# Performance work log

Hardware: AMD Instinct MI355X
Metric: run time of the kernel (lower is better)

Reference implementation:

```python
import jax, jax.numpy as jnp
import numpy as np

B, S, D, H = 4, 1024, 1024, 16
HD = D // H  # head_dim = 64


def setup_inputs() -> dict:
    key = jax.random.key(0)
    ks = jax.random.split(key, 16)
    w = lambda k: jax.random.normal(k, (D, D), dtype=jnp.float32) * 0.02
    b = lambda k: jax.random.normal(k, (D,), dtype=jnp.float32) * 0.02
    x = jax.random.normal(ks[0], (B, S, D), dtype=jnp.float32)
    mask = jnp.tril(jnp.ones((S, S), dtype=jnp.int32))[None, None]  # causal [1,1,S,S]
    bar_indices = jax.random.randint(ks[1], (S,), 0, S, dtype=jnp.int64)
    beat_indices = jax.random.randint(ks[2], (S,), 0, S, dtype=jnp.int64)
    return {
        "x": x, "mask": mask, "bar_indices": bar_indices, "beat_indices": beat_indices,
        "Wq": w(ks[3]), "bq": b(ks[4]), "Wk": w(ks[5]), "bk": b(ks[6]),
        "Wv": w(ks[7]), "bv": b(ks[8]),
        "W_bark": w(ks[9]), "b_bark": b(ks[10]),
        "W_beatk": w(ks[11]), "b_beatk": b(ks[12]),
        "Wo": w(ks[13]), "bo": b(ks[14]),
    }


def reference(x, mask, bar_indices, beat_indices, Wq, bq, Wk, bk, Wv, bv,
              W_bark, b_bark, W_beatk, b_beatk, Wo, bo):
    Bs, Sl, Dm = x.shape
    heads, hd = H, Dm // H

    def proj(t, W, b):  # torch Linear: t @ W.T + b, then split heads -> [B,H,S,hd]
        y = t @ W.T + b
        return y.reshape(Bs, -1, heads, hd).transpose(0, 2, 1, 3)

    q = proj(x, Wq, bq)
    k = proj(x, Wk, bk)
    v = proj(x, Wv, bv)
    scale = 1.0 / jnp.sqrt(jnp.asarray(hd, x.dtype))

    scores = jnp.einsum('bhqd,bhkd->bhqk', q, k) * scale

    # hierarchical bar bias (bar_query is computed but unused in the original)
    bar_k = proj(x[:, bar_indices], W_bark, b_bark)
    scores = scores + 0.2 * (jnp.einsum('bhqd,bhkd->bhqk', q, bar_k) * scale)

    # hierarchical beat bias
    beat_k = proj(x[:, beat_indices], W_beatk, b_beatk)
    scores = scores + 0.1 * (jnp.einsum('bhqd,bhkd->bhqk', q, beat_k) * scale)

    scores = jnp.where(mask == 0, jnp.asarray(-1e9, scores.dtype), scores)
    attn = jax.nn.softmax(scores, axis=-1)  # dropout is identity in eval

    out = jnp.einsum('bhqk,bhkd->bhqd', attn, v)
    out = out.transpose(0, 2, 1, 3).reshape(Bs, Sl, Dm)
    return out @ Wo.T + bo
```

## Files before the change

### kernel.cpp

```cpp
#include <hip/hip_runtime.h>
#include <hip/hip_bf16.h>


typedef __bf16 bf16x8 __attribute__((ext_vector_type(8)));
typedef __bf16 bf16x4 __attribute__((ext_vector_type(4)));
typedef float  f32x4  __attribute__((ext_vector_type(4)));

#define DMODEL 1024

#define ASYNC_LOAD16(gp, lp)                                                  \
    __builtin_amdgcn_global_load_lds(                                         \
        (const __attribute__((address_space(1))) unsigned int*)(gp),          \
        (__attribute__((address_space(3))) unsigned int*)(lp), 16, 0, 0)

__global__ __launch_bounds__(256) void cvt_kernel(
    const float* __restrict__ x,
    const float* __restrict__ Wq, const float* __restrict__ Wk,
    const float* __restrict__ Wv, const float* __restrict__ Wbar,
    const float* __restrict__ Wbeat, const float* __restrict__ Wo,
    __bf16* __restrict__ dst)
{
    const int g = blockIdx.x * 256 + threadIdx.x;
    const size_t e = (size_t)g * 8;
    const int seg = (int)(e >> 20);
    const float* src; size_t off; float s = 1.0f;
    if (seg < 4)       { src = x;     off = e; }
    else if (seg == 4) { src = Wq;    off = e - ((size_t)4 << 20); }
    else if (seg == 5) { src = Wk;    off = e - ((size_t)5 << 20); }
    else if (seg == 6) { src = Wv;    off = e - ((size_t)6 << 20); }
    else if (seg == 7) { src = Wbar;  off = e - ((size_t)7 << 20); s = 0.2f; }
    else if (seg == 8) { src = Wbeat; off = e - ((size_t)8 << 20); s = 0.1f; }
    else               { src = Wo;    off = e - ((size_t)9 << 20); }
    const float4 a = *(const float4*)&src[off];
    const float4 b = *(const float4*)&src[off + 4];
    bf16x8 v;
    v[0] = (__bf16)(a.x * s); v[1] = (__bf16)(a.y * s);
    v[2] = (__bf16)(a.z * s); v[3] = (__bf16)(a.w * s);
    v[4] = (__bf16)(b.x * s); v[5] = (__bf16)(b.y * s);
    v[6] = (__bf16)(b.z * s); v[7] = (__bf16)(b.w * s);
    *(bf16x8*)&dst[e] = v;
}

__global__ __launch_bounds__(256) void proj_kernel(
    const __bf16* __restrict__ xb, const __bf16* __restrict__ attnbuf,
    const __bf16* __restrict__ Wqb, const __bf16* __restrict__ Wkb,
    const __bf16* __restrict__ Wvb, const __bf16* __restrict__ Wbarb,
    const __bf16* __restrict__ Wbeatb, const __bf16* __restrict__ Wob,
    const float* __restrict__ bq, const float* __restrict__ bk,
    const float* __restrict__ bv, const float* __restrict__ bbar,
    const float* __restrict__ bbeat, const float* __restrict__ bo,
    const int* __restrict__ bar_idx, const int* __restrict__ beat_idx,
    __bf16* __restrict__ qbuf, __bf16* __restrict__ keffbuf,
    __bf16* __restrict__ vtbuf, float* __restrict__ outbuf,
    int mode_base)
{
    const int mode = mode_base + blockIdx.y;
    const int tile = blockIdx.x;
    const int m0 = (tile >> 3) << 7;
    const int n0 = (tile & 7) << 7;

    __shared__ __align__(16) __bf16 Alds[128 * 32];
    __shared__ __align__(16) __bf16 Blds[128 * 32];

    const int t    = threadIdx.x;
    const int w    = t >> 6;
    const int lane = t & 63;
    const int l15  = lane & 15;
    const int quad = lane >> 4;
    const int wm   = (w >> 1) << 6;
    const int wn   = (w & 1) << 6;
    const int srow = t >> 2;
    const int scol = (t & 3) * 8;

    const __bf16* Aptr = (mode == 3) ? attnbuf : xb;
    const int nterms = (mode == 1) ? 3 : 1;

    f32x4 acc[4][4];
    for (int i = 0; i < 4; ++i)
        for (int j = 0; j < 4; ++j)
            acc[i][j] = {0.f, 0.f, 0.f, 0.f};

    for (int term = 0; term < nterms; ++term) {
        const __bf16* Wterm =
            (mode == 0) ? Wqb :
            (mode == 2) ? Wvb :
            (mode == 3) ? Wob :
            (term == 0) ? Wkb : (term == 1) ? Wbarb : Wbeatb;

        int arow0, arow1;
        if (mode != 1 || term == 0) {
            arow0 = m0 + srow;
            arow1 = m0 + 64 + srow;
        } else {
            const int* gi = (term == 1) ? bar_idx : beat_idx;
            const int bbase = m0 & ~1023;
            arow0 = bbase + gi[(m0 & 1023) + srow];
            arow1 = bbase + gi[(m0 & 1023) + 64 + srow];
        }
        const __bf16* gA0 = Aptr + (size_t)arow0 * DMODEL + scol;
        const __bf16* gA1 = Aptr + (size_t)arow1 * DMODEL + scol;
        const __bf16* gB0 = Wterm + (size_t)(n0 + srow) * DMODEL + scol;
        const __bf16* gB1 = Wterm + (size_t)(n0 + 64 + srow) * DMODEL + scol;
        __bf16* lA0 = &Alds[w * 512];
        __bf16* lA1 = &Alds[2048 + w * 512];
        __bf16* lB0 = &Blds[w * 512];
        __bf16* lB1 = &Blds[2048 + w * 512];

        for (int kk = 0; kk < 32; ++kk) {
            const int k0 = kk * 32;
            ASYNC_LOAD16(gA0 + k0, lA0);
            ASYNC_LOAD16(gA1 + k0, lA1);
            ASYNC_LOAD16(gB0 + k0, lB0);
            ASYNC_LOAD16(gB1 + k0, lB1);
            __syncthreads();

            bf16x8 af[4], bfr[4];
            for (int i = 0; i < 4; ++i)
                af[i] = *(const bf16x8*)&Alds[(wm + i * 16 + l15) * 32 + quad * 8];
            for (int j = 0; j < 4; ++j)
                bfr[j] = *(const bf16x8*)&Blds[(wn + j * 16 + l15) * 32 + quad * 8];

            for (int i = 0; i < 4; ++i)
                for (int j = 0; j < 4; ++j)
                    acc[i][j] = __builtin_amdgcn_mfma_f32_16x16x32_bf16(
                        af[i], bfr[j], acc[i][j], 0, 0, 0);
            __syncthreads();
        }
    }

    for (int j = 0; j < 4; ++j) {
        const int col = n0 + wn + j * 16 + l15;
        float bias;
        if (mode == 0)      bias = bq[col];
        else if (mode == 1) bias = bk[col] + 0.2f * bbar[col] + 0.1f * bbeat[col];
        else if (mode == 2) bias = bv[col];
        else                bias = bo[col];

        for (int i = 0; i < 4; ++i) {
            const int rowbase = m0 + wm + i * 16 + quad * 4;
            if (mode == 2) {
                const int bb = rowbase >> 10;
                const int sb = rowbase & 1023;
                bf16x4 vv;
                for (int r = 0; r < 4; ++r) vv[r] = (__bf16)(acc[i][j][r] + bias);
                *(bf16x4*)&vtbuf[((size_t)(bb * 1024 + col)) * 1024 + sb] = vv;
            } else if (mode == 3) {
                for (int r = 0; r < 4; ++r)
                    outbuf[(size_t)(rowbase + r) * DMODEL + col] =
                        acc[i][j][r] + bias;
            } else if (mode == 0) {
                for (int r = 0; r < 4; ++r)
                    qbuf[(size_t)(rowbase + r) * DMODEL + col] =
                        (__bf16)((acc[i][j][r] + bias) * 0.125f);
            } else {
                for (int r = 0; r < 4; ++r)
                    keffbuf[(size_t)(rowbase + r) * DMODEL + col] =
                        (__bf16)(acc[i][j][r] + bias);
            }
        }
    }
}

__global__ __launch_bounds__(256) void oproj_kernel(
    const __bf16* __restrict__ attnb, const __bf16* __restrict__ Wob,
    const float* __restrict__ bo, float* __restrict__ outb)
{
    const int tile = blockIdx.x;
    const int m0 = (tile >> 3) << 6;
    const int n0 = (tile & 7) << 7;

    __shared__ __align__(16) __bf16 Alds[64 * 32];
    __shared__ __align__(16) __bf16 Blds[128 * 32];

    const int t    = threadIdx.x;
    const int w    = t >> 6;
    const int lane = t & 63;
    const int l15  = lane & 15;
    const int quad = lane >> 4;
    const int wm   = (w >> 1) << 5;
    const int wn   = (w & 1) << 6;
    const int srow = t >> 2;
    const int scol = (t & 3) * 8;

    const __bf16* gA  = attnb + (size_t)(m0 + srow) * DMODEL + scol;
    const __bf16* gB0 = Wob + (size_t)(n0 + srow) * DMODEL + scol;
    const __bf16* gB1 = Wob + (size_t)(n0 + 64 + srow) * DMODEL + scol;
    __bf16* lA  = &Alds[w * 512];
    __bf16* lB0 = &Blds[w * 512];
    __bf16* lB1 = &Blds[2048 + w * 512];

    f32x4 acc[2][4];
    for (int i = 0; i < 2; ++i)
        for (int j = 0; j < 4; ++j)
            acc[i][j] = {0.f, 0.f, 0.f, 0.f};

    for (int kk = 0; kk < 32; ++kk) {
        const int k0 = kk * 32;
        ASYNC_LOAD16(gA + k0, lA);
        ASYNC_LOAD16(gB0 + k0, lB0);
        ASYNC_LOAD16(gB1 + k0, lB1);
        __syncthreads();

        bf16x8 af[2], bfr[4];
        for (int i = 0; i < 2; ++i)
            af[i] = *(const bf16x8*)&Alds[(wm + i * 16 + l15) * 32 + quad * 8];
        for (int j = 0; j < 4; ++j)
            bfr[j] = *(const bf16x8*)&Blds[(wn + j * 16 + l15) * 32 + quad * 8];

        for (int i = 0; i < 2; ++i)
            for (int j = 0; j < 4; ++j)
                acc[i][j] = __builtin_amdgcn_mfma_f32_16x16x32_bf16(
                    af[i], bfr[j], acc[i][j], 0, 0, 0);
        __syncthreads();
    }

    for (int j = 0; j < 4; ++j) {
        const int col = n0 + wn + j * 16 + l15;
        const float bias = bo[col];
        for (int i = 0; i < 2; ++i) {
            const int rowbase = m0 + wm + i * 16 + quad * 4;
            for (int r = 0; r < 4; ++r)
                outb[(size_t)(rowbase + r) * DMODEL + col] = acc[i][j][r] + bias;
        }
    }
}

__global__ __launch_bounds__(256) void attn_kernel(
    const __bf16* __restrict__ qbuf, const __bf16* __restrict__ keffbuf,
    const __bf16* __restrict__ vtbuf, __bf16* __restrict__ attnbuf)
{
    const int bh = blockIdx.y;
    const int b  = bh >> 4;
    const int h  = bh & 15;
    const int qt = blockIdx.x;
    const int q0 = qt * 64;

    __shared__ __align__(16) __bf16 Klds[64][72];
    __shared__ __align__(16) __bf16 Vlds[64][72];
    __shared__ __align__(16) __bf16 Plds[4][16][72];

    const int t    = threadIdx.x;
    const int w    = t >> 6;
    const int lane = t & 63;
    const int l15  = lane & 15;
    const int quad = lane >> 4;

    const __bf16* qbase =
        qbuf + (size_t)(b * 1024 + q0 + w * 16 + l15) * DMODEL + h * 64;
    bf16x8 qf0 = *(const bf16x8*)&qbase[quad * 8];
    bf16x8 qf1 = *(const bf16x8*)&qbase[32 + quad * 8];

    bf16x8 ones;
    for (int i = 0; i < 8; ++i) ones[i] = (__bf16)1.0f;

    f32x4 o[4];
    for (int i = 0; i < 4; ++i) o[i] = {0.f, 0.f, 0.f, 0.f};
    f32x4 lacc = {0.f, 0.f, 0.f, 0.f};

    const int srow = t >> 2;
    const int scol = (t & 3) * 16;

    const __bf16* kbase = keffbuf + (size_t)(b * 1024) * DMODEL + h * 64;
    const __bf16* vtb   = vtbuf + (size_t)(b * 1024 + h * 64) * 1024;

    for (int j = 0; j <= qt; ++j) {
        const __bf16* kg = kbase + (size_t)(j * 64 + srow) * DMODEL + scol;
        *(bf16x8*)&Klds[srow][scol]     = *(const bf16x8*)kg;
        *(bf16x8*)&Klds[srow][scol + 8] = *(const bf16x8*)(kg + 8);
        const __bf16* vg = vtb + (size_t)srow * 1024 + j * 64 + scol;
        *(bf16x8*)&Vlds[srow][scol]     = *(const bf16x8*)vg;
        *(bf16x8*)&Vlds[srow][scol + 8] = *(const bf16x8*)(vg + 8);
        __syncthreads();

        f32x4 sc[4];
        for (int nt = 0; nt < 4; ++nt) {
            sc[nt] = {0.f, 0.f, 0.f, 0.f};
            bf16x8 kf0 = *(const bf16x8*)&Klds[nt * 16 + l15][quad * 8];
            bf16x8 kf1 = *(const bf16x8*)&Klds[nt * 16 + l15][32 + quad * 8];
            sc[nt] = __builtin_amdgcn_mfma_f32_16x16x32_bf16(qf0, kf0, sc[nt], 0, 0, 0);
            sc[nt] = __builtin_amdgcn_mfma_f32_16x16x32_bf16(qf1, kf1, sc[nt], 0, 0, 0);
        }

        if (j == qt) {
            const int qrow_base = q0 + w * 16 + quad * 4;
            for (int nt = 0; nt < 4; ++nt) {
                const int kcol = j * 64 + nt * 16 + l15;
                for (int r = 0; r < 4; ++r)
                    if (kcol > qrow_base + r) sc[nt][r] = -1e30f;
            }
        }

        for (int nt = 0; nt < 4; ++nt)
            for (int r = 0; r < 4; ++r)
                sc[nt][r] = __expf(sc[nt][r]);

        for (int nt = 0; nt < 4; ++nt)
            for (int r = 0; r < 4; ++r)
                Plds[w][quad * 4 + r][nt * 16 + l15] = (__bf16)sc[nt][r];
        asm volatile("s_waitcnt lgkmcnt(0)" ::: "memory");

        bf16x8 pf0 = *(const bf16x8*)&Plds[w][l15][quad * 8];
        bf16x8 pf1 = *(const bf16x8*)&Plds[w][l15][32 + quad * 8];

        lacc = __builtin_amdgcn_mfma_f32_16x16x32_bf16(pf0, ones, lacc, 0, 0, 0);
        lacc = __builtin_amdgcn_mfma_f32_16x16x32_bf16(pf1, ones, lacc, 0, 0, 0);

        for (int nd = 0; nd < 4; ++nd) {
            bf16x8 vf0 = *(const bf16x8*)&Vlds[nd * 16 + l15][quad * 8];
            bf16x8 vf1 = *(const bf16x8*)&Vlds[nd * 16 + l15][32 + quad * 8];
            o[nd] = __builtin_amdgcn_mfma_f32_16x16x32_bf16(pf0, vf0, o[nd], 0, 0, 0);
            o[nd] = __builtin_amdgcn_mfma_f32_16x16x32_bf16(pf1, vf1, o[nd], 0, 0, 0);
        }
        __syncthreads();
    }

    float rinv[4];
    for (int r = 0; r < 4; ++r) rinv[r] = 1.0f / lacc[r];
    for (int nd = 0; nd < 4; ++nd) {
        for (int r = 0; r < 4; ++r) {
            const int row = q0 + w * 16 + quad * 4 + r;
            attnbuf[(size_t)(b * 1024 + row) * DMODEL + h * 64 + nd * 16 + l15] =
                (__bf16)(o[nd][r] * rinv[r]);
        }
    }
}

extern "C" void kernel_launch(void* const* d_in, const int* in_sizes, int n_in,
                              void* d_out, int out_size, void* d_ws, size_t ws_size,
                              hipStream_t stream) {
    const float* x     = (const float*)d_in[0];
    const int* bar     = (const int*)d_in[2];
    const int* beat    = (const int*)d_in[3];
    const float* Wq    = (const float*)d_in[4];
    const float* bq    = (const float*)d_in[5];
    const float* Wk    = (const float*)d_in[6];
    const float* bk    = (const float*)d_in[7];
    const float* Wv    = (const float*)d_in[8];
    const float* bv    = (const float*)d_in[9];
    const float* Wbar  = (const float*)d_in[10];
    const float* bbar  = (const float*)d_in[11];
    const float* Wbeat = (const float*)d_in[12];
    const float* bbeat = (const float*)d_in[13];
    const float* Wo    = (const float*)d_in[14];
    const float* bo    = (const float*)d_in[15];

    const size_t M1 = (size_t)1 << 20;
    __bf16* xb     = (__bf16*)d_ws;
    __bf16* Wqb    = xb + 4 * M1;
    __bf16* Wkb    = Wqb + M1;
    __bf16* Wvb    = Wkb + M1;
    __bf16* Wbarb  = Wvb + M1;
    __bf16* Wbeatb = Wbarb + M1;
    __bf16* Wob    = Wbeatb + M1;
    __bf16* qbuf   = Wob + M1;
    __bf16* keff   = qbuf + 4 * M1;
    __bf16* vt     = keff + 4 * M1;
    __bf16* attn   = vt + 4 * M1;
    float*  outb   = (float*)d_out;

    cvt_kernel<<<5120, 256, 0, stream>>>(x, Wq, Wk, Wv, Wbar, Wbeat, Wo, xb);

    proj_kernel<<<dim3(256, 3), 256, 0, stream>>>(
        xb, attn, Wqb, Wkb, Wvb, Wbarb, Wbeatb, Wob,
        bq, bk, bv, bbar, bbeat, bo, bar, beat,
        qbuf, keff, vt, outb, 0);

    attn_kernel<<<dim3(16, 64), 256, 0, stream>>>(qbuf, keff, vt, attn);

    oproj_kernel<<<512, 256, 0, stream>>>(attn, Wob, bo, outb);
}
```

Measured before the change: 237.5 us.

## Replace projection GEMM with double-buffered 8-wave 128x256 tile kernel

Swaps the simple single-buffered 128x128 projection GEMM for a 512-thread kernel with 128x256 tiles, BK=64, double-buffered LDS, XOR-swizzled layout and a four-phase interleaving of async global-to-LDS loads with MFMA bursts. Longer-running K-effective blocks (48 k-steps) are scheduled first. The goal is to hide global memory latency, cut LDS bank conflicts and per-kstep barrier overhead in the Q/Keff/V projections. It relies on hand-placed vmcnt waits and barriers being correct, and uses much more LDS per block (96 KB), which may limit occupancy.

```diff
diff --git a/kernel.cpp b/kernel.cpp
--- a/kernel.cpp
+++ b/kernel.cpp
@@ -41,121 +41,235 @@
     *(bf16x8*)&dst[e] = v;
 }
 
-__global__ __launch_bounds__(256) void proj_kernel(
-    const __bf16* __restrict__ xb, const __bf16* __restrict__ attnbuf,
+
+#define SWZ_COL(r_, ks_) \
+    (((((ks_) * 64) + quad * 16) ^ ((((r_) >> 2) & 1) << 5)) >> 1)
+
+#define READ_A(c_, mh_)                                                       \
+    do {                                                                      \
+        _Pragma("unroll") for (int mi = 0; mi < 2; ++mi) {                    \
+            const int r_ = ((w >> 2) << 5) + (mh_) * 64 + mi * 16 + l15;      \
+            _Pragma("unroll") for (int ks = 0; ks < 2; ++ks)                  \
+                af[mi][ks] = *(const bf16x8*)&Alds[(c_) * 8192 + r_ * 64 +    \
+                                                   SWZ_COL(r_, ks)];          \
+        }                                                                     \
+    } while (0)
+
+#define READ_B(c_, nh_)                                                       \
+    do {                                                                      \
+        _Pragma("unroll") for (int nj = 0; nj < 2; ++nj) {                    \
+            const int r_ = ((w & 3) << 5) + (nh_) * 128 + nj * 16 + l15;      \
+            _Pragma("unroll") for (int ks = 0; ks < 2; ++ks)                  \
+                bf[nj][ks] = *(const bf16x8*)&Blds[(c_) * 16384 + r_ * 64 +   \
+                                                    SWZ_COL(r_, ks)];         \
+        }                                                                     \
+    } while (0)
+
+#define STAGE_A8(bufn_, h_, kt_)                                              \
+    do {                                                                      \
+        const int tm_ = (kt_) >> 4;                                           \
+        const int k0_ = ((kt_) & 15) << 6;                                    \
+        const __bf16* ap_ = (tm_ == 0) ? aA0##h_ : (tm_ == 1) ? aA1##h_       \
+                                                              : aA2##h_;      \
+        ASYNC_LOAD16(ap_ + k0_,                                               \
+                     &Alds[(bufn_) * 8192 + (h_) * 4096 + w * 512]);          \
+    } while (0)
+
+#define STAGE_B8(bufn_, h_, kt_)                                              \
+    do {                                                                      \
+        const int tm_ = (kt_) >> 4;                                           \
+        const int k0_ = ((kt_) & 15) << 6;                                    \
+        const __bf16* wp_ = (tm_ == 0) ? W0 : (tm_ == 1) ? W1 : W2;           \
+        ASYNC_LOAD16(wp_ + bro##h_##0 + k0_,                                  \
+                     &Blds[(bufn_) * 16384 + (h_) * 8192 + w * 512]);         \
+        ASYNC_LOAD16(wp_ + bro##h_##1 + k0_,                                  \
+                     &Blds[(bufn_) * 16384 + (h_) * 8192 + 4096 + w * 512]);  \
+    } while (0)
+
+#define PHASE_BAR1()                                                          \
+    do {                                                                      \
+        __builtin_amdgcn_s_barrier();                                         \
+        asm volatile("s_waitcnt lgkmcnt(0)" ::: "memory");                    \
+    } while (0)
+
+#define MFMA8(mh_, nh_)                                                       \
+    do {                                                                      \
+        __builtin_amdgcn_s_setprio(1);                                        \
+        _Pragma("unroll") for (int mi = 0; mi < 2; ++mi)                      \
+        _Pragma("unroll") for (int nj = 0; nj < 2; ++nj) {                    \
+            acc[(mh_)*2 + mi][(nh_)*2 + nj] =                                 \
+                __builtin_amdgcn_mfma_f32_16x16x32_bf16(                      \
+                    af[mi][0], bf[nj][0], acc[(mh_)*2 + mi][(nh_)*2 + nj],    \
+                    0, 0, 0);                                                 \
+            acc[(mh_)*2 + mi][(nh_)*2 + nj] =                                 \
+                __builtin_amdgcn_mfma_f32_16x16x32_bf16(                      \
+                    af[mi][1], bf[nj][1], acc[(mh_)*2 + mi][(nh_)*2 + nj],    \
+                    0, 0, 0);                                                 \
+        }                                                                     \
+        __builtin_amdgcn_s_setprio(0);                                        \
+    } while (0)
+
+__global__ __launch_bounds__(512, 2) void gemm8p_kernel(
+    const __bf16* __restrict__ xb,
     const __bf16* __restrict__ Wqb, const __bf16* __restrict__ Wkb,
     const __bf16* __restrict__ Wvb, const __bf16* __restrict__ Wbarb,
-    const __bf16* __restrict__ Wbeatb, const __bf16* __restrict__ Wob,
+    const __bf16* __restrict__ Wbeatb,
     const float* __restrict__ bq, const float* __restrict__ bk,
     const float* __restrict__ bv, const float* __restrict__ bbar,
-    const float* __restrict__ bbeat, const float* __restrict__ bo,
+    const float* __restrict__ bbeat,
     const int* __restrict__ bar_idx, const int* __restrict__ beat_idx,
     __bf16* __restrict__ qbuf, __bf16* __restrict__ keffbuf,
-    __bf16* __restrict__ vtbuf, float* __restrict__ outbuf,
-    int mode_base)
+    __bf16* __restrict__ vtbuf)
 {
-    const int mode = mode_base + blockIdx.y;
-    const int tile = blockIdx.x;
-    const int m0 = (tile >> 3) << 7;
-    const int n0 = (tile & 7) << 7;
-
-    __shared__ __align__(16) __bf16 Alds[128 * 32];
-    __shared__ __align__(16) __bf16 Blds[128 * 32];
-
-    const int t    = threadIdx.x;
+    __shared__ __align__(16) __bf16 Alds[2 * 8192];
+    __shared__ __align__(16) __bf16 Blds[2 * 16384];
+
+    const int bid = blockIdx.x;
+    int mode, tk;
+    if (bid < 128)      { mode = 1; tk = bid; }
+    else if (bid < 256) { mode = 0; tk = bid - 128; }
+    else                { mode = 2; tk = bid - 256; }
+    const int m0 = (tk >> 2) << 7;
+    const int n0 = (tk & 3) << 8;
+    const int nkt = (mode == 1) ? 48 : 16;
+
+    const int t    = (int)threadIdx.x;
     const int w    = t >> 6;
     const int lane = t & 63;
     const int l15  = lane & 15;
     const int quad = lane >> 4;
-    const int wm   = (w >> 1) << 6;
-    const int wn   = (w & 1) << 6;
-    const int srow = t >> 2;
-    const int scol = (t & 3) * 8;
-
-    const __bf16* Aptr = (mode == 3) ? attnbuf : xb;
-    const int nterms = (mode == 1) ? 3 : 1;
+
+    const int srow = t >> 3;
+    const int scol = ((((t & 7) * 16) ^ (((t >> 5) & 1) << 5)) >> 1);
+
+    const __bf16* aA00 = xb + (size_t)(m0 + srow) * DMODEL + scol;
+    const __bf16* aA01 = xb + (size_t)(m0 + 64 + srow) * DMODEL + scol;
+    const __bf16* aA10 = aA00; const __bf16* aA11 = aA01;
+    const __bf16* aA20 = aA00; const __bf16* aA21 = aA01;
+    const __bf16 *W0, *W1, *W2;
+    if (mode == 0)      { W0 = W1 = W2 = Wqb; }
+    else if (mode == 2) { W0 = W1 = W2 = Wvb; }
+    else {
+        W0 = Wkb; W1 = Wbarb; W2 = Wbeatb;
+        const int bb = m0 & ~1023;
+        const int lr = m0 & 1023;
+        aA10 = xb + (size_t)(bb + bar_idx[lr + srow]) * DMODEL + scol;
+        aA11 = xb + (size_t)(bb + bar_idx[lr + 64 + srow]) * DMODEL + scol;
+        aA20 = xb + (size_t)(bb + beat_idx[lr + srow]) * DMODEL + scol;
+        aA21 = xb + (size_t)(bb + beat_idx[lr + 64 + srow]) * DMODEL + scol;
+    }
+    const size_t bro00 = (size_t)(n0 + srow) * DMODEL + scol;
+    const size_t bro01 = (size_t)(n0 + 64 + srow) * DMODEL + scol;
+    const size_t bro10 = (size_t)(n0 + 128 + srow) * DMODEL + scol;
+    const size_t bro11 = (size_t)(n0 + 192 + srow) * DMODEL + scol;
 
     f32x4 acc[4][4];
+#pragma unroll
     for (int i = 0; i < 4; ++i)
+#pragma unroll
         for (int j = 0; j < 4; ++j)
             acc[i][j] = {0.f, 0.f, 0.f, 0.f};
-
-    for (int term = 0; term < nterms; ++term) {
-        const __bf16* Wterm =
-            (mode == 0) ? Wqb :
-            (mode == 2) ? Wvb :
-            (mode == 3) ? Wob :
-            (term == 0) ? Wkb : (term == 1) ? Wbarb : Wbeatb;
-
-        int arow0, arow1;
-        if (mode != 1 || term == 0) {
-            arow0 = m0 + srow;
-            arow1 = m0 + 64 + srow;
-        } else {
-            const int* gi = (term == 1) ? bar_idx : beat_idx;
-            const int bbase = m0 & ~1023;
-            arow0 = bbase + gi[(m0 & 1023) + srow];
-            arow1 = bbase + gi[(m0 & 1023) + 64 + srow];
-        }
-        const __bf16* gA0 = Aptr + (size_t)arow0 * DMODEL + scol;
-        const __bf16* gA1 = Aptr + (size_t)arow1 * DMODEL + scol;
-        const __bf16* gB0 = Wterm + (size_t)(n0 + srow) * DMODEL + scol;
-        const __bf16* gB1 = Wterm + (size_t)(n0 + 64 + srow) * DMODEL + scol;
-        __bf16* lA0 = &Alds[w * 512];
-        __bf16* lA1 = &Alds[2048 + w * 512];
-        __bf16* lB0 = &Blds[w * 512];
-        __bf16* lB1 = &Blds[2048 + w * 512];
-
-        for (int kk = 0; kk < 32; ++kk) {
-            const int k0 = kk * 32;
-            ASYNC_LOAD16(gA0 + k0, lA0);
-            ASYNC_LOAD16(gA1 + k0, lA1);
-            ASYNC_LOAD16(gB0 + k0, lB0);
-            ASYNC_LOAD16(gB1 + k0, lB1);
-            __syncthreads();
-
-            bf16x8 af[4], bfr[4];
-            for (int i = 0; i < 4; ++i)
-                af[i] = *(const bf16x8*)&Alds[(wm + i * 16 + l15) * 32 + quad * 8];
-            for (int j = 0; j < 4; ++j)
-                bfr[j] = *(const bf16x8*)&Blds[(wn + j * 16 + l15) * 32 + quad * 8];
-
-            for (int i = 0; i < 4; ++i)
-                for (int j = 0; j < 4; ++j)
-                    acc[i][j] = __builtin_amdgcn_mfma_f32_16x16x32_bf16(
-                        af[i], bfr[j], acc[i][j], 0, 0, 0);
-            __syncthreads();
-        }
-    }
-
-    for (int j = 0; j < 4; ++j) {
-        const int col = n0 + wn + j * 16 + l15;
+    bf16x8 af[2][2], bf[2][2];
+
+    STAGE_A8(0, 0, 0);
+    asm volatile("" ::: "memory");
+    STAGE_B8(0, 0, 0);
+    asm volatile("" ::: "memory");
+    STAGE_B8(0, 1, 0);
+    asm volatile("" ::: "memory");
+    STAGE_A8(0, 1, 0);
+    asm volatile("s_waitcnt vmcnt(3)" ::: "memory");
+    __builtin_amdgcn_s_barrier();
+
+#pragma unroll 1
+    for (int kt = 0; kt < nkt - 1; ++kt) {
+        const int c  = kt & 1;
+        const int nb = c ^ 1;
+        const int kn = kt + 1;
+
+        READ_A(c, 0);
+        READ_B(c, 0);
+        STAGE_A8(nb, 0, kn);
+        PHASE_BAR1();
+        MFMA8(0, 0);
+        asm volatile("s_waitcnt vmcnt(2)" ::: "memory");
+        __builtin_amdgcn_s_barrier();
+
+        READ_B(c, 1);
+        STAGE_B8(nb, 0, kn);
+        PHASE_BAR1();
+        MFMA8(0, 1);
+        asm volatile("s_waitcnt vmcnt(3)" ::: "memory");
+        __builtin_amdgcn_s_barrier();
+
+        READ_A(c, 1);
+        STAGE_B8(nb, 1, kn);
+        PHASE_BAR1();
+        MFMA8(1, 1);
+        __builtin_amdgcn_s_barrier();
+
+        READ_B(c, 0);
+        STAGE_A8(nb, 1, kn);
+        PHASE_BAR1();
+        MFMA8(1, 0);
+        asm volatile("s_waitcnt vmcnt(3)" ::: "memory");
+        __builtin_amdgcn_s_barrier();
+    }
+
+    {
+        const int c = (nkt - 1) & 1;
+        READ_A(c, 0);
+        READ_B(c, 0);
+        PHASE_BAR1();
+        MFMA8(0, 0);
+        asm volatile("s_waitcnt vmcnt(1)" ::: "memory");
+        __builtin_amdgcn_s_barrier();
+
+        READ_B(c, 1);
+        PHASE_BAR1();
+        MFMA8(0, 1);
+        asm volatile("s_waitcnt vmcnt(0)" ::: "memory");
+        __builtin_amdgcn_s_barrier();
+
+        READ_A(c, 1);
+        PHASE_BAR1();
+        MFMA8(1, 1);
+        __builtin_amdgcn_s_barrier();
+
+        READ_B(c, 0);
+        PHASE_BAR1();
+        MFMA8(1, 0);
+    }
+
+#pragma unroll
+    for (int an = 0; an < 4; ++an) {
+        const int col = n0 + ((w & 3) << 5) + (an >> 1) * 128 +
+                        (an & 1) * 16 + l15;
         float bias;
         if (mode == 0)      bias = bq[col];
         else if (mode == 1) bias = bk[col] + 0.2f * bbar[col] + 0.1f * bbeat[col];
-        else if (mode == 2) bias = bv[col];
-        else                bias = bo[col];
-
-        for (int i = 0; i < 4; ++i) {
-            const int rowbase = m0 + wm + i * 16 + quad * 4;
+        else                bias = bv[col];
+#pragma unroll
+        for (int am = 0; am < 4; ++am) {
+            const int rowbase = m0 + ((w >> 2) << 5) + (am >> 1) * 64 +
+                                (am & 1) * 16 + quad * 4;
             if (mode == 2) {
                 const int bb = rowbase >> 10;
                 const int sb = rowbase & 1023;
                 bf16x4 vv;
-                for (int r = 0; r < 4; ++r) vv[r] = (__bf16)(acc[i][j][r] + bias);
+#pragma unroll
+                for (int r = 0; r < 4; ++r) vv[r] = (__bf16)(acc[am][an][r] + bias);
                 *(bf16x4*)&vtbuf[((size_t)(bb * 1024 + col)) * 1024 + sb] = vv;
-            } else if (mode == 3) {
-                for (int r = 0; r < 4; ++r)
-                    outbuf[(size_t)(rowbase + r) * DMODEL + col] =
-                        acc[i][j][r] + bias;
             } else if (mode == 0) {
+#pragma unroll
                 for (int r = 0; r < 4; ++r)
                     qbuf[(size_t)(rowbase + r) * DMODEL + col] =
-                        (__bf16)((acc[i][j][r] + bias) * 0.125f);
+                        (__bf16)((acc[am][an][r] + bias) * 0.125f);
             } else {
+#pragma unroll
                 for (int r = 0; r < 4; ++r)
                     keffbuf[(size_t)(rowbase + r) * DMODEL + col] =
-                        (__bf16)(acc[i][j][r] + bias);
+                        (__bf16)(acc[am][an][r] + bias);
             }
         }
     }
@@ -360,10 +474,10 @@
 
     cvt_kernel<<<5120, 256, 0, stream>>>(x, Wq, Wk, Wv, Wbar, Wbeat, Wo, xb);
 
-    proj_kernel<<<dim3(256, 3), 256, 0, stream>>>(
-        xb, attn, Wqb, Wkb, Wvb, Wbarb, Wbeatb, Wob,
-        bq, bk, bv, bbar, bbeat, bo, bar, beat,
-        qbuf, keff, vt, outb, 0);
+    gemm8p_kernel<<<384, 512, 0, stream>>>(
+        xb, Wqb, Wkb, Wvb, Wbarb, Wbeatb,
+        bq, bk, bv, bbar, bbeat, bar, beat,
+        qbuf, keff, vt);
 
     attn_kernel<<<dim3(16, 64), 256, 0, stream>>>(qbuf, keff, vt, attn);
 
```

Result: slower. 244.8 us (+3.1%).
